# Kernel optimization log

Measured on AMD Instinct MI355X. Metric: run time of the kernel, lower is better.

## Reference

```python
import jax, jax.numpy as jnp
import numpy as np

B, T, I, H, O = 4096, 512, 1, 50, 1


def setup_inputs() -> dict:
    key = jax.random.key(0)
    ks = jax.random.split(key, 7)
    s = 1.0 / np.sqrt(H)  # torch LSTM/Linear default init scale
    x = jax.random.normal(ks[0], (B, T, I), dtype=jnp.float32)
    W_ih = jax.random.uniform(ks[1], (4 * H, I), jnp.float32, -s, s)
    W_hh = jax.random.uniform(ks[2], (4 * H, H), jnp.float32, -s, s)
    b_ih = jax.random.uniform(ks[3], (4 * H,), jnp.float32, -s, s)
    b_hh = jax.random.uniform(ks[4], (4 * H,), jnp.float32, -s, s)
    W_fc = jax.random.uniform(ks[5], (O, H), jnp.float32, -s, s)
    b_fc = jax.random.uniform(ks[6], (O,), jnp.float32, -s, s)
    return {"x": x, "W_ih": W_ih, "W_hh": W_hh, "b_ih": b_ih,
            "b_hh": b_hh, "W_fc": W_fc, "b_fc": b_fc}


def reference(x, W_ih, W_hh, b_ih, b_hh, W_fc, b_fc):
    # x: [B, T, I]. Precompute input projections for all timesteps: [B, T, 4H]
    xp = jnp.einsum('bti,gi->btg', x, W_ih) + (b_ih + b_hh)

    def step(carry, xt):
        h, c = carry  # [B, H] each
        gates = xt + h @ W_hh.T  # [B, 4H]; torch gate order: i, f, g, o
        i, f, g, o = jnp.split(gates, 4, axis=-1)
        c = jax.nn.sigmoid(f) * c + jax.nn.sigmoid(i) * jnp.tanh(g)
        h = jax.nn.sigmoid(o) * jnp.tanh(c)
        return (h, c), None

    h0 = jnp.zeros((x.shape[0], W_hh.shape[1]), x.dtype)
    (h_last, _), _ = jax.lax.scan(step, (h0, h0), jnp.swapaxes(xp, 0, 1))
    # final-timestep hidden -> Linear
    return h_last @ W_fc.T + b_fc  # [B, O]
```

## Files before the change

### kernel.cpp

```cpp
#include <hip/hip_runtime.h>
#include <math.h>

#define T_LEN 512
#define H_DIM 50
#define BPB   16
#define L2E   1.44269504088896f
#define HSTR  88
#define XSTR  520

typedef _Float16 half8_t __attribute__((ext_vector_type(8)));
typedef float    f32x4_t __attribute__((ext_vector_type(4)));

__device__ __forceinline__ f32x4_t mfma16(half8_t a, half8_t b, f32x4_t c) {
#if defined(__HIP_DEVICE_COMPILE__)
    return __builtin_amdgcn_mfma_f32_16x16x32_f16(a, b, c, 0, 0, 0);
#else
    return c;
#endif
}

__device__ __forceinline__ int pk16(float a, float b) {
    return __builtin_bit_cast(int, __builtin_amdgcn_cvt_pkrtz(a, b));
}

__device__ __forceinline__ float sigm(float v) {
    return __builtin_amdgcn_rcpf(1.0f + __builtin_amdgcn_exp2f(v * (-L2E)));
}
__device__ __forceinline__ float tanh_f(float v) {
    return __fmaf_rn(
        __builtin_amdgcn_rcpf(1.0f + __builtin_amdgcn_exp2f(v * (-2.0f * L2E))),
        2.0f, -1.0f);
}

__global__ __launch_bounds__(512, 1) void lstm_mfma(
    const float* __restrict__ x,
    const float* __restrict__ W_ih,
    const float* __restrict__ W_hh,
    const float* __restrict__ b_ih,
    const float* __restrict__ b_hh,
    const float* __restrict__ W_fc,
    const float* __restrict__ b_fc,
    float* __restrict__ out)
{
    const int tid = threadIdx.x;
    const int w   = tid >> 6;
    const int L   = tid & 63;
    const int col = L & 15;
    const int g4  = L >> 4;

    __shared__ _Float16 xls[BPB][XSTR];
    __shared__ _Float16 hls[2][BPB][HSTR];

    {
        const float4* xg4 = reinterpret_cast<const float4*>(
            x + (size_t)blockIdx.x * BPB * T_LEN);
        #pragma unroll
        for (int r = 0; r < 4; ++r) {
            const int f = tid + 512 * r;
            const float4 v = xg4[f];
            const int bb = f >> 7;
            const int c0 = (f & 127) << 2;
            *reinterpret_cast<int*>(&xls[bb][c0])     = pk16(v.x, v.y);
            *reinterpret_cast<int*>(&xls[bb][c0 + 2]) = pk16(v.z, v.w);
        }
    }
    {
        int* hz = reinterpret_cast<int*>(hls);
        for (int i = tid; i < 2 * BPB * HSTR / 2; i += 512) hz[i] = 0;
    }
    __syncthreads();
    if (tid < BPB) {
        hls[0][tid][50] = xls[tid][0];
        hls[0][tid][51] = (_Float16)1.0f;
        hls[1][tid][51] = (_Float16)1.0f;
    }

    const int m0 = (w < 5) ? 2 * w     : (w + 5);
    const int m1 = (w < 5) ? 2 * w + 1 : (w + 8);

    auto load_frag = [&](int m, int kc) -> half8_t {
        const int p = 16 * m + col;
        const int u = p >> 2, gg = p & 3;
        half8_t h8;
        #pragma unroll
        for (int j = 0; j < 8; ++j) {
            const int k = 32 * kc + 8 * g4 + j;
            float v = 0.0f;
            if (u < H_DIM) {
                const int r = gg * H_DIM + u;
                if (k < H_DIM)     v = W_hh[r * H_DIM + k];
                else if (k == 50)  v = W_ih[r];
                else if (k == 51)  v = b_ih[r] + b_hh[r];
            }
            h8[j] = (_Float16)v;
        }
        return h8;
    };
    const half8_t a00 = load_frag(m0, 0), a01 = load_frag(m0, 1);
    const half8_t a10 = load_frag(m1, 0), a11 = load_frag(m1, 1);

    const int u0  = 4 * m0 + g4;
    const int u1  = 4 * m1 + g4;
    const bool wr0 = (u0 < H_DIM);
    const bool wr1 = (u1 < H_DIM);
    const bool xw  = (w == 7) && (L < BPB);

    float c0 = 0.0f, c1 = 0.0f;
    const f32x4_t zero4 = {0.0f, 0.0f, 0.0f, 0.0f};
    __syncthreads();

    #pragma unroll 2
    for (int t = 0; t < T_LEN; ++t) {
        const int cur = t & 1, nxt = cur ^ 1;
        const half8_t b0 = *reinterpret_cast<const half8_t*>(&hls[cur][col][8 * g4]);
        const half8_t b1 = *reinterpret_cast<const half8_t*>(&hls[cur][col][32 + 8 * g4]);

        f32x4_t acc0 = mfma16(a00, b0, zero4);
        f32x4_t acc1 = mfma16(a10, b0, zero4);
        acc0 = mfma16(a01, b1, acc0);
        acc1 = mfma16(a11, b1, acc1);

        {
            const float ig = sigm(acc0[0]);
            const float fg = sigm(acc0[1]);
            const float gt = tanh_f(acc0[2]);
            const float og = sigm(acc0[3]);
            c0 = __fmaf_rn(fg, c0, ig * gt);
            const float hv = og * tanh_f(c0);
            if (wr0) hls[nxt][col][u0] = (_Float16)hv;
        }
        {
            const float ig = sigm(acc1[0]);
            const float fg = sigm(acc1[1]);
            const float gt = tanh_f(acc1[2]);
            const float og = sigm(acc1[3]);
            c1 = __fmaf_rn(fg, c1, ig * gt);
            const float hv = og * tanh_f(c1);
            if (wr1) hls[nxt][col][u1] = (_Float16)hv;
        }
        if (xw) hls[nxt][L][50] = xls[L][t + 1];
        __syncthreads();
    }

    if (w == 0) {
        float part = 0.0f;
        #pragma unroll
        for (int j = 0; j < 13; ++j) {
            const int u = 13 * g4 + j;
            if (u < H_DIM) part += (float)hls[0][col][u] * W_fc[u];
        }
        part += __shfl_xor(part, 16);
        part += __shfl_xor(part, 32);
        if (L < BPB) out[blockIdx.x * BPB + L] = part + b_fc[0];
    }
}

extern "C" void kernel_launch(void* const* d_in, const int* in_sizes, int n_in,
                              void* d_out, int out_size, void* d_ws, size_t ws_size,
                              hipStream_t stream) {
    const float* x    = (const float*)d_in[0];
    const float* W_ih = (const float*)d_in[1];
    const float* W_hh = (const float*)d_in[2];
    const float* b_ih = (const float*)d_in[3];
    const float* b_hh = (const float*)d_in[4];
    const float* W_fc = (const float*)d_in[5];
    const float* b_fc = (const float*)d_in[6];
    float* out = (float*)d_out;

    const int B = in_sizes[0] / T_LEN;
    lstm_mfma<<<dim3(B / BPB), dim3(512), 0, stream>>>(
        x, W_ih, W_hh, b_ih, b_hh, W_fc, b_fc, out);
}
```

Baseline: 207.3 us.

## Use 13 waves with one MFMA tile each, bias in accumulator, blocked h layout

```diff
diff --git a/kernel.cpp b/kernel.cpp
--- a/kernel.cpp
+++ b/kernel.cpp
@@ -4,8 +4,8 @@
 #define T_LEN 512
 #define H_DIM 50
 #define BPB   16
+#define NW    13
 #define L2E   1.44269504088896f
-#define HSTR  88
 #define XSTR  520
 
 typedef _Float16 half8_t __attribute__((ext_vector_type(8)));
@@ -18,11 +18,9 @@
     return c;
 #endif
 }
-
 __device__ __forceinline__ int pk16(float a, float b) {
     return __builtin_bit_cast(int, __builtin_amdgcn_cvt_pkrtz(a, b));
 }
-
 __device__ __forceinline__ float sigm(float v) {
     return __builtin_amdgcn_rcpf(1.0f + __builtin_amdgcn_exp2f(v * (-L2E)));
 }
@@ -32,7 +30,7 @@
         2.0f, -1.0f);
 }
 
-__global__ __launch_bounds__(512, 1) void lstm_mfma(
+__global__ __launch_bounds__(NW * 64, 1) void lstm_mfma(
     const float* __restrict__ x,
     const float* __restrict__ W_ih,
     const float* __restrict__ W_hh,
@@ -49,14 +47,12 @@
     const int g4  = L >> 4;
 
     __shared__ _Float16 xls[BPB][XSTR];
-    __shared__ _Float16 hls[2][BPB][HSTR];
+    __shared__ __align__(16) _Float16 hb[2][8][BPB][8];
 
     {
         const float4* xg4 = reinterpret_cast<const float4*>(
             x + (size_t)blockIdx.x * BPB * T_LEN);
-        #pragma unroll
-        for (int r = 0; r < 4; ++r) {
-            const int f = tid + 512 * r;
+        for (int f = tid; f < BPB * T_LEN / 4; f += NW * 64) {
             const float4 v = xg4[f];
             const int bb = f >> 7;
             const int c0 = (f & 127) << 2;
@@ -64,81 +60,57 @@
             *reinterpret_cast<int*>(&xls[bb][c0 + 2]) = pk16(v.z, v.w);
         }
     }
-    {
-        int* hz = reinterpret_cast<int*>(hls);
-        for (int i = tid; i < 2 * BPB * HSTR / 2; i += 512) hz[i] = 0;
-    }
+    for (int i = tid; i < 1024; i += NW * 64) reinterpret_cast<int*>(hb)[i] = 0;
     __syncthreads();
-    if (tid < BPB) {
-        hls[0][tid][50] = xls[tid][0];
-        hls[0][tid][51] = (_Float16)1.0f;
-        hls[1][tid][51] = (_Float16)1.0f;
+    if (tid < BPB) hb[0][6][tid][2] = xls[tid][0];
+
+    const int pA = 16 * w + col;
+    const int uA = pA >> 2, gA = pA & 3;
+    half8_t a0, a1;
+    #pragma unroll
+    for (int j = 0; j < 8; ++j) {
+        const int k0 = 8 * g4 + j;
+        const int k1 = 32 + k0;
+        float v0 = 0.0f, v1 = 0.0f;
+        if (uA < H_DIM) {
+            const int r = gA * H_DIM + uA;
+            v0 = W_hh[r * H_DIM + k0];
+            if (k1 < H_DIM)       v1 = W_hh[r * H_DIM + k1];
+            else if (k1 == H_DIM) v1 = W_ih[r];
+        }
+        a0[j] = (_Float16)v0;
+        a1[j] = (_Float16)v1;
     }
 
-    const int m0 = (w < 5) ? 2 * w     : (w + 5);
-    const int m1 = (w < 5) ? 2 * w + 1 : (w + 8);
+    const int uD  = 4 * w + g4;
+    const bool wr = (uD < H_DIM);
+    f32x4_t biasC;
+    #pragma unroll
+    for (int j = 0; j < 4; ++j)
+        biasC[j] = wr ? (b_ih[j * H_DIM + uD] + b_hh[j * H_DIM + uD]) : 0.0f;
+    const int wrblk = uD >> 3, wrslot = uD & 7;
+    const bool xw = (w == 12) && (g4 == 3);
 
-    auto load_frag = [&](int m, int kc) -> half8_t {
-        const int p = 16 * m + col;
-        const int u = p >> 2, gg = p & 3;
-        half8_t h8;
-        #pragma unroll
-        for (int j = 0; j < 8; ++j) {
-            const int k = 32 * kc + 8 * g4 + j;
-            float v = 0.0f;
-            if (u < H_DIM) {
-                const int r = gg * H_DIM + u;
-                if (k < H_DIM)     v = W_hh[r * H_DIM + k];
-                else if (k == 50)  v = W_ih[r];
-                else if (k == 51)  v = b_ih[r] + b_hh[r];
-            }
-            h8[j] = (_Float16)v;
-        }
-        return h8;
-    };
-    const half8_t a00 = load_frag(m0, 0), a01 = load_frag(m0, 1);
-    const half8_t a10 = load_frag(m1, 0), a11 = load_frag(m1, 1);
-
-    const int u0  = 4 * m0 + g4;
-    const int u1  = 4 * m1 + g4;
-    const bool wr0 = (u0 < H_DIM);
-    const bool wr1 = (u1 < H_DIM);
-    const bool xw  = (w == 7) && (L < BPB);
-
-    float c0 = 0.0f, c1 = 0.0f;
-    const f32x4_t zero4 = {0.0f, 0.0f, 0.0f, 0.0f};
+    float c = 0.0f;
     __syncthreads();
 
     #pragma unroll 2
     for (int t = 0; t < T_LEN; ++t) {
         const int cur = t & 1, nxt = cur ^ 1;
-        const half8_t b0 = *reinterpret_cast<const half8_t*>(&hls[cur][col][8 * g4]);
-        const half8_t b1 = *reinterpret_cast<const half8_t*>(&hls[cur][col][32 + 8 * g4]);
+        const half8_t b0 = *reinterpret_cast<const half8_t*>(&hb[cur][g4][col][0]);
+        const half8_t b1 = *reinterpret_cast<const half8_t*>(&hb[cur][4 + g4][col][0]);
 
-        f32x4_t acc0 = mfma16(a00, b0, zero4);
-        f32x4_t acc1 = mfma16(a10, b0, zero4);
-        acc0 = mfma16(a01, b1, acc0);
-        acc1 = mfma16(a11, b1, acc1);
+        f32x4_t acc = mfma16(a0, b0, biasC);
+        acc = mfma16(a1, b1, acc);
 
-        {
-            const float ig = sigm(acc0[0]);
-            const float fg = sigm(acc0[1]);
-            const float gt = tanh_f(acc0[2]);
-            const float og = sigm(acc0[3]);
-            c0 = __fmaf_rn(fg, c0, ig * gt);
-            const float hv = og * tanh_f(c0);
-            if (wr0) hls[nxt][col][u0] = (_Float16)hv;
-        }
-        {
-            const float ig = sigm(acc1[0]);
-            const float fg = sigm(acc1[1]);
-            const float gt = tanh_f(acc1[2]);
-            const float og = sigm(acc1[3]);
-            c1 = __fmaf_rn(fg, c1, ig * gt);
-            const float hv = og * tanh_f(c1);
-            if (wr1) hls[nxt][col][u1] = (_Float16)hv;
-        }
-        if (xw) hls[nxt][L][50] = xls[L][t + 1];
+        const float ig = sigm(acc[0]);
+        const float fg = sigm(acc[1]);
+        const float gt = tanh_f(acc[2]);
+        const float og = sigm(acc[3]);
+        c = __fmaf_rn(fg, c, ig * gt);
+        const float hv = og * tanh_f(c);
+        if (wr) hb[nxt][wrblk][col][wrslot] = (_Float16)hv;
+        if (xw) hb[nxt][6][col][2] = xls[col][t + 1];
         __syncthreads();
     }
 
@@ -147,7 +119,8 @@
         #pragma unroll
         for (int j = 0; j < 13; ++j) {
             const int u = 13 * g4 + j;
-            if (u < H_DIM) part += (float)hls[0][col][u] * W_fc[u];
+            if (u < H_DIM)
+                part += (float)hb[0][u >> 3][col][u & 7] * W_fc[u];
         }
         part += __shfl_xor(part, 16);
         part += __shfl_xor(part, 32);
@@ -168,6 +141,6 @@
     float* out = (float*)d_out;
 
     const int B = in_sizes[0] / T_LEN;
-    lstm_mfma<<<dim3(B / BPB), dim3(512), 0, stream>>>(
+    lstm_mfma<<<dim3(B / BPB), dim3(NW * 64), 0, stream>>>(
         x, W_ih, W_hh, b_ih, b_hh, W_fc, b_fc, out);
 }
```

Measured after the change: 211.1 us. About the same (+1.8%).
